# Kernel tuning notes

Measured on AMD Instinct MI355X. Metric: run time of the kernel, lower is better.

The kernel has to match this reference:

```python
import jax, jax.numpy as jnp
import numpy as np

B, N, IN_DIM = 2, 2048, 1024
HEADS, HEAD_DIM = 16, 64

def setup_inputs() -> dict:
    key = jax.random.key(0)
    k1, k2, k3, k4, k5 = jax.random.split(key, 5)
    s_in = 1.0 / np.sqrt(IN_DIM)
    s_h = 1.0 / np.sqrt(HEADS * HEAD_DIM)
    return {
        "x": jax.random.normal(k1, (B, N, IN_DIM), jnp.float32),
        "w_qkv": jax.random.normal(k2, (IN_DIM, 3 * HEADS * HEAD_DIM), jnp.float32) * s_in,
        "b_qkv": jax.random.normal(k3, (3 * HEADS * HEAD_DIM,), jnp.float32) * s_in,
        "w_proj": jax.random.normal(k4, (HEADS * HEAD_DIM, IN_DIM), jnp.float32) * s_h,
        "b_proj": jax.random.normal(k5, (IN_DIM,), jnp.float32) * s_h,
    }

def reference(x, w_qkv, b_qkv, w_proj, b_proj):
    b, n, _ = x.shape
    scale = HEAD_DIM ** (-0.5)
    qkv = x @ w_qkv + b_qkv                               # (B,N,3*H*D)
    # torch: reshape(B,N,H,3*D).permute(0,2,1,3) then chunk last dim into q,k,v
    qkv = qkv.reshape(b, n, HEADS, 3 * HEAD_DIM).transpose(0, 2, 1, 3)  # (B,H,N,3D)
    q, k, v = jnp.split(qkv, 3, axis=-1)                  # each (B,H,N,D)
    attn = jnp.einsum("bhqd,bhkd->bhqk", q, k) * scale    # (B,H,N,N)
    attn = jax.nn.softmax(attn, axis=-1)
    out = jnp.einsum("bhqk,bhkd->bhqd", attn, v)          # (B,H,N,D)
    out = out.transpose(0, 2, 1, 3).reshape(b, n, HEADS * HEAD_DIM)
    return out @ w_proj + b_proj
```

## Files before the change

kernel.cpp:

```cpp
#include <hip/hip_runtime.h>
#include <hip/hip_bf16.h>
#include <cstdint>
#include <cstddef>

#define BD 2
#define SEQ 2048
#define NH 16
#define HD 64
#define IND 1024
#define QKVD 3072
#define MROWS (BD * SEQ)
#define NT (SEQ / 64)

typedef __attribute__((ext_vector_type(8))) short s8v;
typedef __attribute__((ext_vector_type(4))) short s4v;
typedef __attribute__((ext_vector_type(4))) float f4v;

__device__ __forceinline__ short f2bf(float f) {
  __hip_bfloat16 h = __float2bfloat16(f);
  return *reinterpret_cast<short*>(&h);
}

__device__ __forceinline__ void async_copy16(void* lds, const void* g) {
  __builtin_amdgcn_global_load_lds(
      (const __attribute__((address_space(1))) unsigned int*)g,
      (__attribute__((address_space(3))) unsigned int*)lds, 16, 0, 0);
}

__device__ __forceinline__ const s8v* lds_frag(const short* p, int row, int col) {
  int byte = (row << 7) + (col << 1);
  byte ^= ((row & 7) << 4);
  return (const s8v*)((const char*)p + byte);
}

__global__ void k_cast(const float* __restrict__ in, short* __restrict__ out, int n4) {
  int i = blockIdx.x * blockDim.x + threadIdx.x;
  if (i >= n4) return;
  float4 v = reinterpret_cast<const float4*>(in)[i];
  s4v o;
  o[0] = f2bf(v.x); o[1] = f2bf(v.y); o[2] = f2bf(v.z); o[3] = f2bf(v.w);
  reinterpret_cast<s4v*>(out)[i] = o;
}

__global__ void k_transpose_cast(const float* __restrict__ w, short* __restrict__ wT,
                                 int R, int C) {
  __shared__ float tile[32][33];
  int c0 = blockIdx.x * 32, r0 = blockIdx.y * 32;
  int tx = threadIdx.x, ty = threadIdx.y;
  #pragma unroll
  for (int j = 0; j < 32; j += 8)
    tile[ty + j][tx] = w[(size_t)(r0 + ty + j) * C + c0 + tx];
  __syncthreads();
  #pragma unroll
  for (int j = 0; j < 32; j += 8)
    wT[(size_t)(c0 + ty + j) * R + r0 + tx] = f2bf(tile[tx][ty + j]);
}

template <int MODE>
__global__ __launch_bounds__(256) void k_gemm(const short* __restrict__ A,
                                              const short* __restrict__ BT,
                                              const float* __restrict__ bias,
                                              short* __restrict__ obf,
                                              float* __restrict__ ofl,
                                              int Mr, int Nc, int K) {
  constexpr int BM = 128, BN = 128, BK = 32;
  __shared__ short As[BM][BK];
  __shared__ short Bs[BN][BK];
  const int rm = blockIdx.x * BM, cn = blockIdx.y * BN;
  const int t = threadIdx.x, l = t & 63;
  const int wm = (t >> 6) >> 1, wn = (t >> 6) & 1;
  const int lr = l & 15, lc = l >> 4;

  f4v acc[4][4];
  #pragma unroll
  for (int m = 0; m < 4; ++m)
    #pragma unroll
    for (int n = 0; n < 4; ++n) acc[m][n] = (f4v)0.0f;

  for (int k0 = 0; k0 < K; k0 += BK) {
    __syncthreads();
    #pragma unroll
    for (int p = 0; p < 2; ++p) {
      int c = p * 256 + t;
      async_copy16(&As[c >> 2][(c & 3) * 8],
                   &A[(size_t)(rm + (c >> 2)) * K + k0 + (c & 3) * 8]);
      async_copy16(&Bs[c >> 2][(c & 3) * 8],
                   &BT[(size_t)(cn + (c >> 2)) * K + k0 + (c & 3) * 8]);
    }
    __syncthreads();
    s8v af[4], bf[4];
    #pragma unroll
    for (int m = 0; m < 4; ++m)
      af[m] = *(const s8v*)&As[wm * 64 + m * 16 + lr][lc * 8];
    #pragma unroll
    for (int n = 0; n < 4; ++n)
      bf[n] = *(const s8v*)&Bs[wn * 64 + n * 16 + lr][lc * 8];
    #pragma unroll
    for (int m = 0; m < 4; ++m)
      #pragma unroll
      for (int n = 0; n < 4; ++n)
        acc[m][n] = __builtin_amdgcn_mfma_f32_16x16x32_bf16(af[m], bf[n], acc[m][n], 0, 0, 0);
  }

  const int row0 = rm + wm * 64, col0 = cn + wn * 64;
  #pragma unroll
  for (int n = 0; n < 4; ++n) {
    const int col = col0 + n * 16 + lr;
    const float bv = bias[col];
    if (MODE == 0) {
      const int h = col / 192, rem = col % 192;
      const int wch = rem >> 6, d = rem & 63;
      const float scale = (wch == 0) ? 0.125f : 1.0f;
      short* dst = obf + (size_t)wch * ((size_t)BD * NH * SEQ * HD);
      #pragma unroll
      for (int m = 0; m < 4; ++m)
        #pragma unroll
        for (int r = 0; r < 4; ++r) {
          const int row = row0 + m * 16 + lc * 4 + r;
          const int b = row >> 11, nn = row & (SEQ - 1);
          const short val = f2bf((acc[m][n][r] + bv) * scale);
          if (wch == 2)
            dst[((size_t)(b * NH + h) * HD + d) * SEQ + nn] = val;
          else
            dst[((size_t)(b * NH + h) * SEQ + nn) * HD + d] = val;
        }
    } else {
      #pragma unroll
      for (int m = 0; m < 4; ++m)
        #pragma unroll
        for (int r = 0; r < 4; ++r) {
          const int row = row0 + m * 16 + lc * 4 + r;
          ofl[(size_t)row * Nc + col] = acc[m][n][r] + bv;
        }
    }
  }
}

__global__ __launch_bounds__(256) void k_attn(const short* __restrict__ Qw,
                                              const short* __restrict__ Kw,
                                              const short* __restrict__ Vt_g,
                                              short* __restrict__ AO) {
  const int qb = blockIdx.x, bh = blockIdx.y;
  const size_t base = (size_t)bh * SEQ * HD;
  const int t = threadIdx.x, l = t & 63, w = t >> 6;
  const int lr = l & 15, lc = l >> 4;
  __shared__ short Ks[2][64 * 64];
  __shared__ short Vt[2][64 * 64];
  __shared__ short Ps[4][16 * 64];
  const int q0 = qb * 64 + w * 16;

  int ldsOff[2], kOff[2], vOff[2];
  #pragma unroll
  for (int p = 0; p < 2; ++p) {
    const int c = p * 256 + t;
    const int row = c >> 3, ch = (c & 7) ^ (row & 7);
    ldsOff[p] = c * 16;
    kOff[p] = row * HD + ch * 8;
    vOff[p] = row * SEQ + ch * 8;
  }
  const short* Kb = Kw + base;
  const short* Vb = Vt_g + base;

  s8v qf[2];
  #pragma unroll
  for (int s = 0; s < 2; ++s)
    qf[s] = *(const s8v*)&Qw[base + (size_t)(q0 + lr) * HD + s * 32 + lc * 8];

  f4v of[4];
  #pragma unroll
  for (int j = 0; j < 4; ++j) of[j] = (f4v)0.0f;
  float Mx = -3.0e38f, Ls = 0.0f;
  short* Pw = &Ps[w][0];

  auto STAGE = [&](int buf, int tile) {
    const size_t kv = (size_t)tile * 64;
    #pragma unroll
    for (int p = 0; p < 2; ++p)
      async_copy16((char*)Ks[buf] + ldsOff[p], Kb + kv * HD + kOff[p]);
    #pragma unroll
    for (int p = 0; p < 2; ++p)
      async_copy16((char*)Vt[buf] + ldsOff[p], Vb + kv + vOff[p]);
  };

  auto COMPUTE = [&](const short* ksB, const short* vtB) {
    f4v st[4];
    #pragma unroll
    for (int j = 0; j < 4; ++j) st[j] = (f4v)0.0f;
    #pragma unroll
    for (int j = 0; j < 4; ++j)
      #pragma unroll
      for (int s = 0; s < 2; ++s) {
        s8v kf = *lds_frag(ksB, j * 16 + lr, s * 32 + lc * 8);
        st[j] = __builtin_amdgcn_mfma_f32_16x16x32_bf16(kf, qf[s], st[j], 0, 0, 0);
      }

    float pm = -3.0e38f;
    #pragma unroll
    for (int j = 0; j < 4; ++j)
      #pragma unroll
      for (int r = 0; r < 4; ++r) pm = fmaxf(pm, st[j][r]);
    pm = fmaxf(pm, __shfl_xor(pm, 16));
    pm = fmaxf(pm, __shfl_xor(pm, 32));
    const float Mn = fmaxf(Mx, pm);
    const float alpha = __expf(Mx - Mn);
    float rs = 0.0f;
    #pragma unroll
    for (int j = 0; j < 4; ++j) {
      s4v pk;
      #pragma unroll
      for (int r = 0; r < 4; ++r) {
        const float p = __expf(st[j][r] - Mn);
        rs += p;
        pk[r] = f2bf(p);
      }
      int byte = (lr << 7) + ((j * 16 + lc * 4) << 1);
      byte ^= ((lr & 7) << 4);
      *(s4v*)((char*)Pw + byte) = pk;
    }
    rs += __shfl_xor(rs, 16);
    rs += __shfl_xor(rs, 32);
    Ls = Ls * alpha + rs;
    Mx = Mn;

    float al[4];
    #pragma unroll
    for (int r = 0; r < 4; ++r) al[r] = __shfl(alpha, lc * 4 + r);
    #pragma unroll
    for (int jd = 0; jd < 4; ++jd)
      #pragma unroll
      for (int r = 0; r < 4; ++r) of[jd][r] *= al[r];

    asm volatile("s_waitcnt lgkmcnt(0)" ::: "memory");

    #pragma unroll
    for (int s = 0; s < 2; ++s) {
      s8v pf = *lds_frag(Pw, lr, s * 32 + lc * 8);
      #pragma unroll
      for (int jd = 0; jd < 4; ++jd) {
        s8v vf = *lds_frag(vtB, jd * 16 + lr, s * 32 + lc * 8);
        of[jd] = __builtin_amdgcn_mfma_f32_16x16x32_bf16(pf, vf, of[jd], 0, 0, 0);
      }
    }
  };

  STAGE(0, 0);
  __syncthreads();
  int cur = 0;
  for (int tt = 0; tt < NT - 1; ++tt) {
    STAGE(cur ^ 1, tt + 1);
    COMPUTE(Ks[cur], Vt[cur]);
    __syncthreads();
    cur ^= 1;
  }
  COMPUTE(Ks[cur], Vt[cur]);

  float li[4];
  #pragma unroll
  for (int r = 0; r < 4; ++r) li[r] = 1.0f / __shfl(Ls, lc * 4 + r);
  const int b = bh >> 4, h = bh & 15;
  #pragma unroll
  for (int jd = 0; jd < 4; ++jd)
    #pragma unroll
    for (int r = 0; r < 4; ++r) {
      const int nq = q0 + lc * 4 + r;
      AO[(size_t)(b * SEQ + nq) * (NH * HD) + h * HD + jd * 16 + lr] =
          f2bf(of[jd][r] * li[r]);
    }
}

extern "C" void kernel_launch(void* const* d_in, const int* in_sizes, int n_in,
                              void* d_out, int out_size, void* d_ws, size_t ws_size,
                              hipStream_t stream) {
  const float* x      = (const float*)d_in[0];
  const float* w_qkv  = (const float*)d_in[1];
  const float* b_qkv  = (const float*)d_in[2];
  const float* w_proj = (const float*)d_in[3];
  const float* b_proj = (const float*)d_in[4];
  float* out = (float*)d_out;

  char* ws = (char*)d_ws;
  short* xb  = (short*)(ws);
  short* wqT = (short*)(ws + 8388608);
  short* wpT = (short*)(ws + 14680064);
  short* Qw  = (short*)(ws + 16777216);
  short* Kw  = (short*)(ws + 25165824);
  short* Vtg = (short*)(ws + 33554432);
  short* AO  = (short*)(ws + 41943040);

  k_cast<<<(MROWS * IND / 4 + 255) / 256, 256, 0, stream>>>(x, xb, MROWS * IND / 4);
  dim3 tb(32, 8);
  k_transpose_cast<<<dim3(QKVD / 32, IND / 32), tb, 0, stream>>>(w_qkv, wqT, IND, QKVD);
  k_transpose_cast<<<dim3(IND / 32, IND / 32), tb, 0, stream>>>(w_proj, wpT, IND, IND);

  k_gemm<0><<<dim3(MROWS / 128, QKVD / 128), 256, 0, stream>>>(
      xb, wqT, b_qkv, Qw, nullptr, MROWS, QKVD, IND);
  k_attn<<<dim3(SEQ / 64, BD * NH), 256, 0, stream>>>(Qw, Kw, Vtg, AO);
  k_gemm<1><<<dim3(MROWS / 128, IND / 128), 256, 0, stream>>>(
      AO, wpT, b_proj, nullptr, out, MROWS, IND, IND);
}
```

Measured before the change: 155.9 us.

## Process two 16-row query tiles per wave in attention kernel

Each wave now handles two query sub-tiles (128 queries per block instead of 64), so every K and V fragment loaded from LDS feeds two MFMAs, and each staged K/V tile is shared by twice as many queries. The aim is to halve global K/V traffic per query and the LDS reads per MFMA. In exchange the grid shrinks to 512 blocks, which may underfill the GPU's CUs, and register pressure roughly doubles for the accumulators and scores, which can lower occupancy.

```diff
diff --git a/kernel.cpp b/kernel.cpp
--- a/kernel.cpp
+++ b/kernel.cpp
@@ -146,8 +146,8 @@
   const int lr = l & 15, lc = l >> 4;
   __shared__ short Ks[2][64 * 64];
   __shared__ short Vt[2][64 * 64];
-  __shared__ short Ps[4][16 * 64];
-  const int q0 = qb * 64 + w * 16;
+  __shared__ short Ps[4][2][16 * 64];
+  const int q0 = qb * 128 + w * 16;
 
   int ldsOff[2], kOff[2], vOff[2];
   #pragma unroll
@@ -161,16 +161,19 @@
   const short* Kb = Kw + base;
   const short* Vb = Vt_g + base;
 
-  s8v qf[2];
-  #pragma unroll
-  for (int s = 0; s < 2; ++s)
-    qf[s] = *(const s8v*)&Qw[base + (size_t)(q0 + lr) * HD + s * 32 + lc * 8];
-
-  f4v of[4];
-  #pragma unroll
-  for (int j = 0; j < 4; ++j) of[j] = (f4v)0.0f;
-  float Mx = -3.0e38f, Ls = 0.0f;
-  short* Pw = &Ps[w][0];
+  s8v qf[2][2];
+  #pragma unroll
+  for (int u = 0; u < 2; ++u)
+    #pragma unroll
+    for (int s = 0; s < 2; ++s)
+      qf[u][s] = *(const s8v*)&Qw[base + (size_t)(q0 + u * 64 + lr) * HD + s * 32 + lc * 8];
+
+  f4v of[2][4];
+  #pragma unroll
+  for (int u = 0; u < 2; ++u)
+    #pragma unroll
+    for (int j = 0; j < 4; ++j) of[u][j] = (f4v)0.0f;
+  float Mx[2] = {-3.0e38f, -3.0e38f}, Ls[2] = {0.0f, 0.0f};
 
   auto STAGE = [&](int buf, int tile) {
     const size_t kv = (size_t)tile * 64;
@@ -183,62 +186,74 @@
   };
 
   auto COMPUTE = [&](const short* ksB, const short* vtB) {
-    f4v st[4];
-    #pragma unroll
-    for (int j = 0; j < 4; ++j) st[j] = (f4v)0.0f;
+    f4v st[2][4];
+    #pragma unroll
+    for (int u = 0; u < 2; ++u)
+      #pragma unroll
+      for (int j = 0; j < 4; ++j) st[u][j] = (f4v)0.0f;
     #pragma unroll
     for (int j = 0; j < 4; ++j)
       #pragma unroll
       for (int s = 0; s < 2; ++s) {
         s8v kf = *lds_frag(ksB, j * 16 + lr, s * 32 + lc * 8);
-        st[j] = __builtin_amdgcn_mfma_f32_16x16x32_bf16(kf, qf[s], st[j], 0, 0, 0);
+        #pragma unroll
+        for (int u = 0; u < 2; ++u)
+          st[u][j] = __builtin_amdgcn_mfma_f32_16x16x32_bf16(kf, qf[u][s], st[u][j], 0, 0, 0);
       }
 
-    float pm = -3.0e38f;
-    #pragma unroll
-    for (int j = 0; j < 4; ++j)
-      #pragma unroll
-      for (int r = 0; r < 4; ++r) pm = fmaxf(pm, st[j][r]);
-    pm = fmaxf(pm, __shfl_xor(pm, 16));
-    pm = fmaxf(pm, __shfl_xor(pm, 32));
-    const float Mn = fmaxf(Mx, pm);
-    const float alpha = __expf(Mx - Mn);
-    float rs = 0.0f;
-    #pragma unroll
-    for (int j = 0; j < 4; ++j) {
-      s4v pk;
-      #pragma unroll
-      for (int r = 0; r < 4; ++r) {
-        const float p = __expf(st[j][r] - Mn);
-        rs += p;
-        pk[r] = f2bf(p);
+    #pragma unroll
+    for (int u = 0; u < 2; ++u) {
+      float pm = -3.0e38f;
+      #pragma unroll
+      for (int j = 0; j < 4; ++j)
+        #pragma unroll
+        for (int r = 0; r < 4; ++r) pm = fmaxf(pm, st[u][j][r]);
+      pm = fmaxf(pm, __shfl_xor(pm, 16));
+      pm = fmaxf(pm, __shfl_xor(pm, 32));
+      const float Mn = fmaxf(Mx[u], pm);
+      const float alpha = __expf(Mx[u] - Mn);
+      float rs = 0.0f;
+      #pragma unroll
+      for (int j = 0; j < 4; ++j) {
+        s4v pk;
+        #pragma unroll
+        for (int r = 0; r < 4; ++r) {
+          const float p = __expf(st[u][j][r] - Mn);
+          rs += p;
+          pk[r] = f2bf(p);
+        }
+        int byte = (lr << 7) + ((j * 16 + lc * 4) << 1);
+        byte ^= ((lr & 7) << 4);
+        *(s4v*)((char*)&Ps[w][u][0] + byte) = pk;
       }
-      int byte = (lr << 7) + ((j * 16 + lc * 4) << 1);
-      byte ^= ((lr & 7) << 4);
-      *(s4v*)((char*)Pw + byte) = pk;
+      rs += __shfl_xor(rs, 16);
+      rs += __shfl_xor(rs, 32);
+      Ls[u] = Ls[u] * alpha + rs;
+      Mx[u] = Mn;
+
+      float al[4];
+      #pragma unroll
+      for (int r = 0; r < 4; ++r) al[r] = __shfl(alpha, lc * 4 + r);
+      #pragma unroll
+      for (int jd = 0; jd < 4; ++jd)
+        #pragma unroll
+        for (int r = 0; r < 4; ++r) of[u][jd][r] *= al[r];
     }
-    rs += __shfl_xor(rs, 16);
-    rs += __shfl_xor(rs, 32);
-    Ls = Ls * alpha + rs;
-    Mx = Mn;
-
-    float al[4];
-    #pragma unroll
-    for (int r = 0; r < 4; ++r) al[r] = __shfl(alpha, lc * 4 + r);
-    #pragma unroll
-    for (int jd = 0; jd < 4; ++jd)
-      #pragma unroll
-      for (int r = 0; r < 4; ++r) of[jd][r] *= al[r];
 
     asm volatile("s_waitcnt lgkmcnt(0)" ::: "memory");
 
     #pragma unroll
     for (int s = 0; s < 2; ++s) {
-      s8v pf = *lds_frag(Pw, lr, s * 32 + lc * 8);
+      s8v pf[2];
+      #pragma unroll
+      for (int u = 0; u < 2; ++u)
+        pf[u] = *lds_frag(&Ps[w][u][0], lr, s * 32 + lc * 8);
       #pragma unroll
       for (int jd = 0; jd < 4; ++jd) {
         s8v vf = *lds_frag(vtB, jd * 16 + lr, s * 32 + lc * 8);
-        of[jd] = __builtin_amdgcn_mfma_f32_16x16x32_bf16(pf, vf, of[jd], 0, 0, 0);
+        #pragma unroll
+        for (int u = 0; u < 2; ++u)
+          of[u][jd] = __builtin_amdgcn_mfma_f32_16x16x32_bf16(pf[u], vf, of[u][jd], 0, 0, 0);
       }
     }
   };
@@ -254,18 +269,21 @@
   }
   COMPUTE(Ks[cur], Vt[cur]);
 
-  float li[4];
-  #pragma unroll
-  for (int r = 0; r < 4; ++r) li[r] = 1.0f / __shfl(Ls, lc * 4 + r);
   const int b = bh >> 4, h = bh & 15;
   #pragma unroll
-  for (int jd = 0; jd < 4; ++jd)
-    #pragma unroll
-    for (int r = 0; r < 4; ++r) {
-      const int nq = q0 + lc * 4 + r;
-      AO[(size_t)(b * SEQ + nq) * (NH * HD) + h * HD + jd * 16 + lr] =
-          f2bf(of[jd][r] * li[r]);
-    }
+  for (int u = 0; u < 2; ++u) {
+    float li[4];
+    #pragma unroll
+    for (int r = 0; r < 4; ++r) li[r] = 1.0f / __shfl(Ls[u], lc * 4 + r);
+    #pragma unroll
+    for (int jd = 0; jd < 4; ++jd)
+      #pragma unroll
+      for (int r = 0; r < 4; ++r) {
+        const int nq = q0 + u * 64 + lc * 4 + r;
+        AO[(size_t)(b * SEQ + nq) * (NH * HD) + h * HD + jd * 16 + lr] =
+            f2bf(of[u][jd][r] * li[r]);
+      }
+  }
 }
 
 extern "C" void kernel_launch(void* const* d_in, const int* in_sizes, int n_in,
@@ -294,7 +312,7 @@
 
   k_gemm<0><<<dim3(MROWS / 128, QKVD / 128), 256, 0, stream>>>(
       xb, wqT, b_qkv, Qw, nullptr, MROWS, QKVD, IND);
-  k_attn<<<dim3(SEQ / 64, BD * NH), 256, 0, stream>>>(Qw, Kw, Vtg, AO);
+  k_attn<<<dim3(SEQ / 128, BD * NH), 256, 0, stream>>>(Qw, Kw, Vtg, AO);
   k_gemm<1><<<dim3(MROWS / 128, IND / 128), 256, 0, stream>>>(
       AO, wpT, b_proj, nullptr, out, MROWS, IND, IND);
 }
```

Measured after the change: 159.0 us. +2.0%, slower.
